# Kernel optimization log

Measured on AMD Instinct MI355X. Metric: run time of the kernel, lower is better.

Reference implementation:

```python
import jax, jax.numpy as jnp
import numpy as np

N = 50000      # nodes
E = 800000     # edges
IN = 128       # in_dim
H = 8          # heads
C = 16         # h_dim (per-head out channels)
ED = 16        # edge_dim
G = 1000       # number of graphs
HC = H * C     # 128
EPS = 1e-16    # PyG softmax epsilon


def setup_inputs() -> dict:
    key = jax.random.key(0)
    ks = jax.random.split(key, 32)
    p = lambda i, shape: jax.random.normal(ks[i], shape, jnp.float32) * 0.1
    inp = {
        "x": jax.random.normal(ks[0], (N, IN), jnp.float32),
        "edge_index": jax.random.randint(ks[1], (2, E), 0, N),
        "edge_attr": jax.random.normal(ks[2], (E, ED), jnp.float32),
        "batch": jnp.sort(jax.random.randint(ks[3], (N,), 0, G)),
    }
    dims = [IN, HC, HC]
    for l in range(3):
        d = dims[l]
        inp[f"W{l+1}"] = p(4 + 6 * l, (d, HC))     # lin weight
        inp[f"We{l+1}"] = p(5 + 6 * l, (ED, HC))   # lin_edge weight
        inp[f"as{l+1}"] = p(6 + 6 * l, (H, C))     # att_src
        inp[f"ad{l+1}"] = p(7 + 6 * l, (H, C))     # att_dst
        inp[f"ae{l+1}"] = p(8 + 6 * l, (H, C))     # att_edge
        inp[f"b{l+1}"] = jnp.zeros((HC,), jnp.float32)
    D = 4 * HC  # cat(h1,h2,h3,h_pool_) -> 512
    inp["Wl1"] = p(22, (D, D)); inp["bl1"] = jnp.zeros((D,), jnp.float32)
    inp["Wl2"] = p(23, (D, 1)); inp["bl2"] = jnp.zeros((1,), jnp.float32)
    return inp


def gat_conv(x, src, dst, edge_attr, W, We, a_s, a_d, a_e, b):
    # x: [N, d_in] -> xs: [N, H, C]
    xs = (x @ W).reshape(-1, H, C)
    ea = (edge_attr @ We).reshape(-1, H, C)          # [E, H, C]
    al_src = jnp.sum(xs * a_s, axis=-1)              # [N, H]
    al_dst = jnp.sum(xs * a_d, axis=-1)              # [N, H]
    al_e = jnp.sum(ea * a_e, axis=-1)                # [E, H]
    alpha = al_src[src] + al_dst[dst] + al_e         # [E, H]
    alpha = jax.nn.leaky_relu(alpha, 0.2)
    amax = jax.ops.segment_max(alpha, dst, num_segments=N)
    ex = jnp.exp(alpha - amax[dst])
    denom = jax.ops.segment_sum(ex, dst, num_segments=N)
    alpha = ex / (denom[dst] + EPS)                  # softmax over in-edges of dst
    msg = xs[src] * alpha[..., None]                 # [E, H, C]
    out = jax.ops.segment_sum(msg, dst, num_segments=N)  # [N, H, C]
    return out.reshape(-1, HC) + b


def reference(x, edge_index, edge_attr, batch,
              W1, We1, as1, ad1, ae1, b1,
              W2, We2, as2, ad2, ae2, b2,
              W3, We3, as3, ad3, ae3, b3,
              Wl1, bl1, Wl2, bl2):
    src, dst = edge_index[0], edge_index[1]
    h1 = gat_conv(x, src, dst, edge_attr, W1, We1, as1, ad1, ae1, b1)
    h2 = gat_conv(h1, src, dst, edge_attr, W2, We2, as2, ad2, ae2, b2)
    h3 = gat_conv(h2, src, dst, edge_attr, W3, We3, as3, ad3, ae3, b3)
    # global_add_pool then broadcast back per node (vectorized gather,
    # replacing the original per-node python loop)
    h_pool = jax.ops.segment_sum(h3, batch, num_segments=G)   # [G, HC]
    h_pool_ = h_pool[batch]                                    # [N, HC]
    h = jnp.concatenate([h1, h2, h3, h_pool_], axis=1)         # [N, 4*HC]
    h = jax.nn.leaky_relu(h @ Wl1 + bl1, 0.01)
    return h @ Wl2 + bl2
```

## Files before the change

kernel.cpp:

```cpp
#include <hip/hip_runtime.h>

#define N_NODES 50000
#define N_EDGES 800000
#define N_GRAPH 1000

typedef short bf16x8 __attribute__((ext_vector_type(8)));
typedef float f32x4 __attribute__((ext_vector_type(4)));

__device__ inline short f2b(float f) {
    union { float f; unsigned u; } x; x.f = f;
    unsigned r = x.u + 0x7FFF + ((x.u >> 16) & 1);
    return (short)(r >> 16);
}
__device__ inline float b2f_lo(unsigned v) {
    union { unsigned u; float f; } x; x.u = v << 16; return x.f;
}
__device__ inline float b2f_hi(unsigned v) {
    union { unsigned u; float f; } x; x.u = v & 0xFFFF0000u; return x.f;
}
__device__ inline float b2f_s(short s) {
    union { unsigned u; float f; } x; x.u = ((unsigned)(unsigned short)s) << 16; return x.f;
}
__device__ inline unsigned pack2(short lo, short hi) {
    return ((unsigned)(unsigned short)lo) | (((unsigned)(unsigned short)hi) << 16);
}

__global__ void f2b_bulk(const float* __restrict__ in, short* __restrict__ out, int n4) {
    int t = blockIdx.x * blockDim.x + threadIdx.x;
    if (t >= n4) return;
    float4 v = *(const float4*)(in + (size_t)t * 4);
    *(short4*)(out + (size_t)t * 4) = make_short4(f2b(v.x), f2b(v.y), f2b(v.z), f2b(v.w));
}

__global__ void wbt_k(const float* __restrict__ W, short* __restrict__ WbT) {
    int idx = blockIdx.x * blockDim.x + threadIdx.x;
    int k = idx >> 7, c = idx & 127;
    WbT[(size_t)c * 128 + k] = f2b(W[idx]);
}

__global__ __launch_bounds__(256) void gemm_mfma(const short* __restrict__ Ab,
                                                 const short* __restrict__ WbT,
                                                 float* __restrict__ out,
                                                 short* __restrict__ outb, int nrows) {
    const int tid = threadIdx.x;
    const int n0 = blockIdx.x * 64;
    const int wid = tid >> 6, lane = tid & 63;
    const int lr = lane & 15, kg = lane >> 4;
    const int wr = (wid >> 1) * 32;
    const int wc = (wid & 1) * 64;

    f32x4 acc[2][4] = {};

#pragma unroll
    for (int ks = 0; ks < 4; ks++) {
        const int k0 = ks * 32;
        bf16x8 a[2], b[4];
#pragma unroll
        for (int fm = 0; fm < 2; fm++) {
            int gr = n0 + wr + fm * 16 + lr;
            bf16x8 v = {};
            if (gr < nrows) v = *(const bf16x8*)(Ab + (size_t)gr * 128 + k0 + kg * 8);
            a[fm] = v;
        }
#pragma unroll
        for (int fn = 0; fn < 4; fn++)
            b[fn] = *(const bf16x8*)(WbT + (size_t)(wc + fn * 16 + lr) * 128 + k0 + kg * 8);
#pragma unroll
        for (int fm = 0; fm < 2; fm++)
#pragma unroll
            for (int fn = 0; fn < 4; fn++)
                acc[fm][fn] = __builtin_amdgcn_mfma_f32_16x16x32_bf16(
                    a[fm], b[fn], acc[fm][fn], 0, 0, 0);
    }
#pragma unroll
    for (int fm = 0; fm < 2; fm++) {
#pragma unroll
        for (int r = 0; r < 4; r++) {
            int gr = n0 + wr + fm * 16 + kg * 4 + r;
            if (gr < nrows) {
#pragma unroll
                for (int fn = 0; fn < 4; fn++) {
                    int col = wc + fn * 16 + lr;
                    float z = acc[fm][fn][r];
                    out[(size_t)gr * 128 + col] = z;
                    outb[(size_t)gr * 128 + col] = f2b(z);
                }
            }
        }
    }
}

__global__ void node_al(const float* __restrict__ xs, const float* __restrict__ a_s,
                        const float* __restrict__ a_d, float* __restrict__ alsrc,
                        float* __restrict__ aldst, int n) {
    int t = blockIdx.x * blockDim.x + threadIdx.x;
    if (t >= n * 8) return;
    int node = t >> 3, h = t & 7;
    const float4* xp = (const float4*)(xs + (size_t)node * 128 + h * 16);
    const float4* sp = (const float4*)(a_s + h * 16);
    const float4* dp = (const float4*)(a_d + h * 16);
    float ss = 0.f, dd = 0.f;
#pragma unroll
    for (int q = 0; q < 4; q++) {
        float4 x4 = xp[q], s4 = sp[q], d4 = dp[q];
        ss += x4.x * s4.x + x4.y * s4.y + x4.z * s4.z + x4.w * s4.w;
        dd += x4.x * d4.x + x4.y * d4.y + x4.z * d4.z + x4.w * d4.w;
    }
    alsrc[t] = ss;
    aldst[t] = dd;
}

__global__ void aew_k(const float* __restrict__ We, const float* __restrict__ ae,
                      float* __restrict__ aeW) {
    int t = threadIdx.x;
    int k = t >> 3, h = t & 7;
    float s = 0.f;
#pragma unroll
    for (int c = 0; c < 16; c++) s += We[k * 128 + h * 16 + c] * ae[h * 16 + c];
    aeW[k * 8 + h] = s;
}

__global__ void hist_k(const int* __restrict__ ei, int* __restrict__ cnt, int ne) {
    int e = blockIdx.x * blockDim.x + threadIdx.x;
    if (e < ne) atomicAdd(&cnt[ei[ne + e]], 1);
}

__global__ void scan1_k(const int* __restrict__ cnt, int* __restrict__ rowptr,
                        int* __restrict__ part, int n) {
    __shared__ int s[256];
    int tid = threadIdx.x;
    int i = blockIdx.x * 256 + tid;
    int v = (i < n) ? cnt[i] : 0;
    s[tid] = v; __syncthreads();
#pragma unroll
    for (int off = 1; off < 256; off <<= 1) {
        int t = (tid >= off) ? s[tid - off] : 0;
        __syncthreads();
        s[tid] += t;
        __syncthreads();
    }
    if (i < n) rowptr[i] = s[tid] - v;
    if (tid == 255) part[blockIdx.x] = s[255];
}

__global__ void scan2_k(int* __restrict__ part, int npart) {
    __shared__ int s[256];
    int tid = threadIdx.x;
    int v = (tid < npart) ? part[tid] : 0;
    s[tid] = v; __syncthreads();
#pragma unroll
    for (int off = 1; off < 256; off <<= 1) {
        int t = (tid >= off) ? s[tid - off] : 0;
        __syncthreads();
        s[tid] += t;
        __syncthreads();
    }
    if (tid < npart) part[tid] = s[tid] - v;
}

__global__ void scan3_k(int* __restrict__ rowptr, const int* __restrict__ part,
                        int* __restrict__ cursor, int n, int ne) {
    int i = blockIdx.x * 256 + threadIdx.x;
    if (i < n) {
        int r = rowptr[i] + part[blockIdx.x];
        rowptr[i] = r;
        cursor[i] = r;
    }
    if (i == 0) rowptr[n] = ne;
}

__global__ void scatter_k(const int* __restrict__ ei, int* __restrict__ cursor,
                          int* __restrict__ pos, int* __restrict__ csr_src, int ne) {
    int e = blockIdx.x * blockDim.x + threadIdx.x;
    if (e >= ne) return;
    int d = ei[ne + e];
    int p = atomicAdd(&cursor[d], 1);
    pos[e] = p;
    csr_src[p] = ei[e];
}

__global__ __launch_bounds__(256) void ale_k(const int* __restrict__ ei,
                                             const float* __restrict__ eattr,
                                             const float* __restrict__ alsrc,
                                             const float* __restrict__ aeW,
                                             const int* __restrict__ pos,
                                             short* __restrict__ aleb, int ne) {
    __shared__ float sAe[128];
    if (threadIdx.x < 128) sAe[threadIdx.x] = aeW[threadIdx.x];
    __syncthreads();
    int e = blockIdx.x * blockDim.x + threadIdx.x;
    if (e >= ne) return;
    float ea[16];
    const float4* ep = (const float4*)(eattr + (size_t)e * 16);
#pragma unroll
    for (int q = 0; q < 4; q++) {
        float4 v = ep[q];
        ea[q * 4 + 0] = v.x; ea[q * 4 + 1] = v.y; ea[q * 4 + 2] = v.z; ea[q * 4 + 3] = v.w;
    }
    int s = ei[e];
    float out[8];
#pragma unroll
    for (int h = 0; h < 8; h++) out[h] = alsrc[s * 8 + h];
#pragma unroll
    for (int k = 0; k < 16; k++)
#pragma unroll
        for (int h = 0; h < 8; h++) out[h] += ea[k] * sAe[k * 8 + h];
    short v8[8];
#pragma unroll
    for (int h = 0; h < 8; h++) v8[h] = f2b(out[h]);
    short* op = aleb + (size_t)pos[e] * 8;
    *(short4*)(op)     = make_short4(v8[0], v8[1], v8[2], v8[3]);
    *(short4*)(op + 4) = make_short4(v8[4], v8[5], v8[6], v8[7]);
}

__global__ __launch_bounds__(256) void gather_k(const int* __restrict__ rowptr,
                                                const int* __restrict__ csr_src,
                                                const short* __restrict__ aleb,
                                                const float* __restrict__ aldst,
                                                const short* __restrict__ xsb,
                                                const float* __restrict__ b,
                                                short* __restrict__ houtb, int n) {
    int dst = blockIdx.x * 4 + (threadIdx.x >> 6);
    if (dst >= n) return;
    const int lane = threadIdx.x & 63;
    const int h = lane >> 3;
    const float L2E = 1.44269504f;
    int p0 = rowptr[dst], p1 = rowptr[dst + 1];
    float ald = aldst[dst * 8 + h];
    float den = 0.f, acc0 = 0.f, acc1 = 0.f;
    int p = p0;
    for (; p + 8 <= p1; p += 8) {
        int   sv  = csr_src[p + (lane & 7)];
        float alv = b2f_s(aleb[(size_t)p * 8 + lane]);
        int s0 = __shfl(sv, 0), s1 = __shfl(sv, 1), s2 = __shfl(sv, 2), s3 = __shfl(sv, 3);
        int s4 = __shfl(sv, 4), s5 = __shfl(sv, 5), s6 = __shfl(sv, 6), s7 = __shfl(sv, 7);
        unsigned v0 = *(const unsigned*)(xsb + (size_t)s0 * 128 + lane * 2);
        unsigned v1 = *(const unsigned*)(xsb + (size_t)s1 * 128 + lane * 2);
        unsigned v2 = *(const unsigned*)(xsb + (size_t)s2 * 128 + lane * 2);
        unsigned v3 = *(const unsigned*)(xsb + (size_t)s3 * 128 + lane * 2);
        unsigned v4 = *(const unsigned*)(xsb + (size_t)s4 * 128 + lane * 2);
        unsigned v5 = *(const unsigned*)(xsb + (size_t)s5 * 128 + lane * 2);
        unsigned v6 = *(const unsigned*)(xsb + (size_t)s6 * 128 + lane * 2);
        unsigned v7 = *(const unsigned*)(xsb + (size_t)s7 * 128 + lane * 2);
        unsigned vv[8] = {v0, v1, v2, v3, v4, v5, v6, v7};
#pragma unroll
        for (int i = 0; i < 8; i++) {
            float al = __shfl(alv, i * 8 + h);
            float lg = al + ald; lg = lg > 0.f ? lg : 0.2f * lg;
            float ex = exp2f(lg * L2E);
            den  += ex;
            acc0 += b2f_lo(vv[i]) * ex;
            acc1 += b2f_hi(vv[i]) * ex;
        }
    }
    for (; p + 1 < p1; p += 2) {
        int s0 = csr_src[p];
        int s1 = csr_src[p + 1];
        float al0 = b2f_s(aleb[(size_t)p * 8 + h]);
        float al1 = b2f_s(aleb[(size_t)(p + 1) * 8 + h]);
        unsigned v0 = *(const unsigned*)(xsb + (size_t)s0 * 128 + lane * 2);
        unsigned v1 = *(const unsigned*)(xsb + (size_t)s1 * 128 + lane * 2);
        float lg0 = al0 + ald; lg0 = lg0 > 0.f ? lg0 : 0.2f * lg0;
        float lg1 = al1 + ald; lg1 = lg1 > 0.f ? lg1 : 0.2f * lg1;
        float ex0 = exp2f(lg0 * L2E);
        float ex1 = exp2f(lg1 * L2E);
        den  += ex0 + ex1;
        acc0 += b2f_lo(v0) * ex0 + b2f_lo(v1) * ex1;
        acc1 += b2f_hi(v0) * ex0 + b2f_hi(v1) * ex1;
    }
    if (p < p1) {
        int s0 = csr_src[p];
        float al0 = b2f_s(aleb[(size_t)p * 8 + h]);
        unsigned v0 = *(const unsigned*)(xsb + (size_t)s0 * 128 + lane * 2);
        float lg0 = al0 + ald; lg0 = lg0 > 0.f ? lg0 : 0.2f * lg0;
        float ex0 = exp2f(lg0 * L2E);
        den  += ex0;
        acc0 += b2f_lo(v0) * ex0;
        acc1 += b2f_hi(v0) * ex0;
    }
    float inv = 1.f / (den + 1e-16f);
    const float2 bb = *(const float2*)(b + lane * 2);
    unsigned o = pack2(f2b(acc0 * inv + bb.x), f2b(acc1 * inv + bb.y));
    *(unsigned*)(houtb + (size_t)dst * 128 + lane * 2) = o;
}

__global__ void pool_k(const short* __restrict__ h3b, const int* __restrict__ batch,
                       float* __restrict__ pool, int n) {
    int t = blockIdx.x * blockDim.x + threadIdx.x;
    if (t >= n * 128) return;
    int node = t >> 7, j = t & 127;
    atomicAdd(pool + (size_t)batch[node] * 128 + j, b2f_s(h3b[t]));
}

__global__ void wl1t_k(const float* __restrict__ Wl1, short* __restrict__ Wl1T) {
    int idx = blockIdx.x * blockDim.x + threadIdx.x;
    int k = idx >> 9, c = idx & 511;
    Wl1T[(size_t)c * 512 + k] = f2b(Wl1[idx]);
}

__global__ void init_out(float* __restrict__ out, const float* __restrict__ bl2, int n) {
    int t = blockIdx.x * blockDim.x + threadIdx.x;
    if (t < n) out[t] = bl2[0];
}

__global__ __launch_bounds__(256) void final_mfma(
    const short* __restrict__ h1, const short* __restrict__ h2,
    const short* __restrict__ h3, const short* __restrict__ poolb,
    const int* __restrict__ batch, const short* __restrict__ Wl1T,
    const float* __restrict__ bl1, const float* __restrict__ Wl2,
    float* __restrict__ out, int nrows)
{
    __shared__ short Abuf[2][4 * 64 * 8];
    __shared__ int   sBatch[64];
    const int tid = threadIdx.x;
    const int n0 = blockIdx.x * 64;
    const int j0 = blockIdx.y * 256;
    const int wid = tid >> 6, lane = tid & 63;
    const int lr = lane & 15, kg = lane >> 4;

    if (tid < 64) {
        int gr = n0 + tid;
        sBatch[tid] = (gr < nrows) ? batch[gr] : 0;
    }
    __syncthreads();

    const short* seg_base[4] = {h1, h2, h3, poolb};

    auto STAGE = [&](int t) {
        const int k0 = t * 32;
        const int seg = k0 >> 7;
        const short* base = seg_base[seg];
        const int cseg = k0 & 127;
        int gr = n0 + lane;
        int grow = (seg == 3) ? sBatch[lane] : ((gr < nrows) ? gr : 0);
        const short* src = base + (size_t)grow * 128 + cseg + wid * 8;
#if __has_builtin(__builtin_amdgcn_global_load_lds)
        __builtin_amdgcn_global_load_lds(
            (const __attribute__((address_space(1))) unsigned int*)src,
            (__attribute__((address_space(3))) unsigned int*)&Abuf[t & 1][(wid * 64 + lane) * 8],
            16, 0, 0);
#else
        uint4 v = *(const uint4*)src;
        *(uint4*)(&Abuf[t & 1][(wid * 64 + lane) * 8]) = v;
#endif
    };
    auto LOADB = [&](int t, bf16x8* bb) {
        const int k0 = t * 32;
#pragma unroll
        for (int fn = 0; fn < 4; fn++)
            bb[fn] = *(const bf16x8*)(Wl1T + (size_t)(j0 + wid * 64 + fn * 16 + lr) * 512
                                      + k0 + kg * 8);
    };

    f32x4 acc[4][4] = {};
    bf16x8 bc[4], bn[4];

    STAGE(0);
    LOADB(0, bc);
    __syncthreads();
#pragma unroll
    for (int t = 0; t < 16; t++) {
        if (t < 15) {
            STAGE(t + 1);
            LOADB(t + 1, bn);
        }
        bf16x8 a[4];
#pragma unroll
        for (int fm = 0; fm < 4; fm++)
            a[fm] = *(const bf16x8*)(&Abuf[t & 1][(kg * 64 + fm * 16 + lr) * 8]);
#pragma unroll
        for (int fm = 0; fm < 4; fm++)
#pragma unroll
            for (int fn = 0; fn < 4; fn++)
                acc[fm][fn] = __builtin_amdgcn_mfma_f32_16x16x32_bf16(
                    a[fm], bc[fn], acc[fm][fn], 0, 0, 0);
        if (t < 15) {
            __syncthreads();
#pragma unroll
            for (int fn = 0; fn < 4; fn++) bc[fn] = bn[fn];
        }
    }

    float w2[4], b1c[4];
#pragma unroll
    for (int fn = 0; fn < 4; fn++) {
        int c = j0 + wid * 64 + fn * 16 + lr;
        w2[fn]  = Wl2[c];
        b1c[fn] = bl1[c];
    }

#pragma unroll
    for (int fm = 0; fm < 4; fm++) {
#pragma unroll
        for (int r = 0; r < 4; r++) {
            float s = 0.f;
#pragma unroll
            for (int fn = 0; fn < 4; fn++) {
                float z = acc[fm][fn][r] + b1c[fn];
                z = z > 0.f ? z : 0.01f * z;
                s += z * w2[fn];
            }
            s += __shfl_xor(s, 1);
            s += __shfl_xor(s, 2);
            s += __shfl_xor(s, 4);
            s += __shfl_xor(s, 8);
            if (lr == 0) {
                int gr = n0 + fm * 16 + kg * 4 + r;
                if (gr < nrows) atomicAdd(out + gr, s);
            }
        }
    }
}

extern "C" void kernel_launch(void* const* d_in, const int* in_sizes, int n_in,
                              void* d_out, int out_size, void* d_ws, size_t ws_size,
                              hipStream_t stream) {
    const float* x     = (const float*)d_in[0];
    const int*   ei    = (const int*)d_in[1];
    const float* eattr = (const float*)d_in[2];
    const int*   batch = (const int*)d_in[3];
    const float* W[3]   = {(const float*)d_in[4],  (const float*)d_in[10], (const float*)d_in[16]};
    const float* We[3]  = {(const float*)d_in[5],  (const float*)d_in[11], (const float*)d_in[17]};
    const float* as_[3] = {(const float*)d_in[6],  (const float*)d_in[12], (const float*)d_in[18]};
    const float* ad_[3] = {(const float*)d_in[7],  (const float*)d_in[13], (const float*)d_in[19]};
    const float* ae_[3] = {(const float*)d_in[8],  (const float*)d_in[14], (const float*)d_in[20]};
    const float* b_[3]  = {(const float*)d_in[9],  (const float*)d_in[15], (const float*)d_in[21]};
    const float* Wl1 = (const float*)d_in[22];
    const float* bl1 = (const float*)d_in[23];
    const float* Wl2 = (const float*)d_in[24];
    const float* bl2 = (const float*)d_in[25];

    const int N = N_NODES, E = N_EDGES, G = N_GRAPH;

    float* ws    = (float*)d_ws;
    float* xs    = ws;
    float* alsrc = xs + (size_t)N * 128;
    float* aldst = alsrc + (size_t)N * 8;
    float* pool  = aldst + (size_t)N * 8;
    float* aeW   = pool + (size_t)G * 128;
    short* xb    = (short*)(aeW + 128);
    short* xsb   = xb + (size_t)N * 128;
    short* hb0   = xsb + (size_t)N * 128;
    short* hb1   = hb0 + (size_t)N * 128;
    short* hb2   = hb1 + (size_t)N * 128;
    short* hb[3] = {hb0, hb1, hb2};
    short* poolb = hb2 + (size_t)N * 128;
    short* wbt0  = poolb + (size_t)G * 128;
    short* wbt1  = wbt0 + 16384;
    short* wbt2  = wbt1 + 16384;
    short* wbt[3] = {wbt0, wbt1, wbt2};
    short* wl1t  = wbt2 + 16384;
    short* aleb  = wl1t + 262144;
    int*   cnt     = (int*)(aleb + (size_t)E * 8);
    int*   rowptr  = cnt + N;
    int*   cursor  = rowptr + N + 1;
    int*   part    = cursor + N;
    int*   pos     = part + 256;
    int*   csr_src = pos + E;

    f2b_bulk<<<(N * 32 + 255) / 256, 256, 0, stream>>>(x, xb, N * 32);
    for (int l = 0; l < 3; l++)
        wbt_k<<<64, 256, 0, stream>>>(W[l], wbt[l]);
    wl1t_k<<<1024, 256, 0, stream>>>(Wl1, wl1t);
    hipMemsetAsync(cnt, 0, (size_t)N * sizeof(int), stream);
    hist_k<<<(E + 255) / 256, 256, 0, stream>>>(ei, cnt, E);
    const int nblk = (N + 255) / 256;
    scan1_k<<<nblk, 256, 0, stream>>>(cnt, rowptr, part, N);
    scan2_k<<<1, 256, 0, stream>>>(part, nblk);
    scan3_k<<<nblk, 256, 0, stream>>>(rowptr, part, cursor, N, E);
    scatter_k<<<(E + 255) / 256, 256, 0, stream>>>(ei, cursor, pos, csr_src, E);

    for (int l = 0; l < 3; l++) {
        const short* Ain = (l == 0) ? xb : hb[l - 1];
        gemm_mfma<<<(N + 63) / 64, 256, 0, stream>>>(Ain, wbt[l], xs, xsb, N);
        node_al<<<(N * 8 + 255) / 256, 256, 0, stream>>>(xs, as_[l], ad_[l], alsrc, aldst, N);
        aew_k<<<1, 128, 0, stream>>>(We[l], ae_[l], aeW);
        ale_k<<<(E + 255) / 256, 256, 0, stream>>>(ei, eattr, alsrc, aeW, pos, aleb, E);
        gather_k<<<(N + 3) / 4, 256, 0, stream>>>(rowptr, csr_src, aleb, aldst, xsb,
                                                  b_[l], hb[l], N);
    }
    hipMemsetAsync(pool, 0, (size_t)G * 128 * sizeof(float), stream);
    pool_k<<<(N * 128 + 255) / 256, 256, 0, stream>>>(hb[2], batch, pool, N);
    f2b_bulk<<<(G * 32 + 255) / 256, 256, 0, stream>>>(pool, poolb, G * 32);

    init_out<<<(N + 255) / 256, 256, 0, stream>>>((float*)d_out, bl2, N);
    dim3 fg((N + 63) / 64, 2);
    final_mfma<<<fg, 256, 0, stream>>>(hb[0], hb[1], hb[2], poolb, batch,
                                       wl1t, bl1, Wl2, (float*)d_out, N);
}
```

Measured before the change: 487.6 us.

## Drop fp32 GEMM output, fold aeW into ale_k, prefetch gather edges

The GEMM now writes only the bf16 projection, and node_al computes attention logits from that bf16 copy. This removes the fp32 store and reload of a 50000x128 buffer in each layer. The tiny aew_k launch is removed by having every ale_k block recompute the 16x8 edge-attention projection into shared memory. The gather loop now software-prefetches the next chunk of source indices and edge logits to hide load latency. The cost is slightly lower precision in the logits and redundant per-block computation of the projection.

```diff
diff --git a/kernel.cpp b/kernel.cpp
--- a/kernel.cpp
+++ b/kernel.cpp
@@ -40,7 +40,6 @@
 
 __global__ __launch_bounds__(256) void gemm_mfma(const short* __restrict__ Ab,
                                                  const short* __restrict__ WbT,
-                                                 float* __restrict__ out,
                                                  short* __restrict__ outb, int nrows) {
     const int tid = threadIdx.x;
     const int n0 = blockIdx.x * 64;
@@ -81,43 +80,32 @@
 #pragma unroll
                 for (int fn = 0; fn < 4; fn++) {
                     int col = wc + fn * 16 + lr;
-                    float z = acc[fm][fn][r];
-                    out[(size_t)gr * 128 + col] = z;
-                    outb[(size_t)gr * 128 + col] = f2b(z);
+                    outb[(size_t)gr * 128 + col] = f2b(acc[fm][fn][r]);
                 }
             }
         }
     }
 }
 
-__global__ void node_al(const float* __restrict__ xs, const float* __restrict__ a_s,
+__global__ void node_al(const short* __restrict__ xsb, const float* __restrict__ a_s,
                         const float* __restrict__ a_d, float* __restrict__ alsrc,
                         float* __restrict__ aldst, int n) {
     int t = blockIdx.x * blockDim.x + threadIdx.x;
     if (t >= n * 8) return;
     int node = t >> 3, h = t & 7;
-    const float4* xp = (const float4*)(xs + (size_t)node * 128 + h * 16);
-    const float4* sp = (const float4*)(a_s + h * 16);
-    const float4* dp = (const float4*)(a_d + h * 16);
+    const short* xp = xsb + (size_t)node * 128 + h * 16;
+    uint4 u0 = *(const uint4*)(xp);
+    uint4 u1 = *(const uint4*)(xp + 8);
+    unsigned w[8] = {u0.x, u0.y, u0.z, u0.w, u1.x, u1.y, u1.z, u1.w};
     float ss = 0.f, dd = 0.f;
 #pragma unroll
-    for (int q = 0; q < 4; q++) {
-        float4 x4 = xp[q], s4 = sp[q], d4 = dp[q];
-        ss += x4.x * s4.x + x4.y * s4.y + x4.z * s4.z + x4.w * s4.w;
-        dd += x4.x * d4.x + x4.y * d4.y + x4.z * d4.z + x4.w * d4.w;
+    for (int q = 0; q < 8; q++) {
+        float lo = b2f_lo(w[q]), hi = b2f_hi(w[q]);
+        ss += lo * a_s[h * 16 + q * 2] + hi * a_s[h * 16 + q * 2 + 1];
+        dd += lo * a_d[h * 16 + q * 2] + hi * a_d[h * 16 + q * 2 + 1];
     }
     alsrc[t] = ss;
     aldst[t] = dd;
-}
-
-__global__ void aew_k(const float* __restrict__ We, const float* __restrict__ ae,
-                      float* __restrict__ aeW) {
-    int t = threadIdx.x;
-    int k = t >> 3, h = t & 7;
-    float s = 0.f;
-#pragma unroll
-    for (int c = 0; c < 16; c++) s += We[k * 128 + h * 16 + c] * ae[h * 16 + c];
-    aeW[k * 8 + h] = s;
 }
 
 __global__ void hist_k(const int* __restrict__ ei, int* __restrict__ cnt, int ne) {
@@ -182,11 +170,18 @@
 __global__ __launch_bounds__(256) void ale_k(const int* __restrict__ ei,
                                              const float* __restrict__ eattr,
                                              const float* __restrict__ alsrc,
-                                             const float* __restrict__ aeW,
+                                             const float* __restrict__ We,
+                                             const float* __restrict__ ae,
                                              const int* __restrict__ pos,
                                              short* __restrict__ aleb, int ne) {
     __shared__ float sAe[128];
-    if (threadIdx.x < 128) sAe[threadIdx.x] = aeW[threadIdx.x];
+    if (threadIdx.x < 128) {
+        int k = threadIdx.x >> 3, h = threadIdx.x & 7;
+        float s = 0.f;
+#pragma unroll
+        for (int c = 0; c < 16; c++) s += We[k * 128 + h * 16 + c] * ae[h * 16 + c];
+        sAe[threadIdx.x] = s;
+    }
     __syncthreads();
     int e = blockIdx.x * blockDim.x + threadIdx.x;
     if (e >= ne) return;
@@ -229,11 +224,22 @@
     float ald = aldst[dst * 8 + h];
     float den = 0.f, acc0 = 0.f, acc1 = 0.f;
     int p = p0;
-    for (; p + 8 <= p1; p += 8) {
-        int   sv  = csr_src[p + (lane & 7)];
-        float alv = b2f_s(aleb[(size_t)p * 8 + lane]);
-        int s0 = __shfl(sv, 0), s1 = __shfl(sv, 1), s2 = __shfl(sv, 2), s3 = __shfl(sv, 3);
-        int s4 = __shfl(sv, 4), s5 = __shfl(sv, 5), s6 = __shfl(sv, 6), s7 = __shfl(sv, 7);
+    const int nfull = (p1 - p0) >> 3;
+    int   sv  = 0;
+    float alv = 0.f;
+    if (nfull > 0) {
+        sv  = csr_src[p + (lane & 7)];
+        alv = b2f_s(aleb[(size_t)p * 8 + lane]);
+    }
+    for (int c = 0; c < nfull; c++) {
+        int csv = sv; float calv = alv;
+        int pn = p + 8;
+        if (c + 1 < nfull) {
+            sv  = csr_src[pn + (lane & 7)];
+            alv = b2f_s(aleb[(size_t)pn * 8 + lane]);
+        }
+        int s0 = __shfl(csv, 0), s1 = __shfl(csv, 1), s2 = __shfl(csv, 2), s3 = __shfl(csv, 3);
+        int s4 = __shfl(csv, 4), s5 = __shfl(csv, 5), s6 = __shfl(csv, 6), s7 = __shfl(csv, 7);
         unsigned v0 = *(const unsigned*)(xsb + (size_t)s0 * 128 + lane * 2);
         unsigned v1 = *(const unsigned*)(xsb + (size_t)s1 * 128 + lane * 2);
         unsigned v2 = *(const unsigned*)(xsb + (size_t)s2 * 128 + lane * 2);
@@ -245,13 +251,14 @@
         unsigned vv[8] = {v0, v1, v2, v3, v4, v5, v6, v7};
 #pragma unroll
         for (int i = 0; i < 8; i++) {
-            float al = __shfl(alv, i * 8 + h);
+            float al = __shfl(calv, i * 8 + h);
             float lg = al + ald; lg = lg > 0.f ? lg : 0.2f * lg;
             float ex = exp2f(lg * L2E);
             den  += ex;
             acc0 += b2f_lo(vv[i]) * ex;
             acc1 += b2f_hi(vv[i]) * ex;
         }
+        p = pn;
     }
     for (; p + 1 < p1; p += 2) {
         int s0 = csr_src[p];
@@ -433,12 +440,10 @@
     const int N = N_NODES, E = N_EDGES, G = N_GRAPH;
 
     float* ws    = (float*)d_ws;
-    float* xs    = ws;
-    float* alsrc = xs + (size_t)N * 128;
+    float* alsrc = ws;
     float* aldst = alsrc + (size_t)N * 8;
     float* pool  = aldst + (size_t)N * 8;
-    float* aeW   = pool + (size_t)G * 128;
-    short* xb    = (short*)(aeW + 128);
+    short* xb    = (short*)(pool + (size_t)G * 128);
     short* xsb   = xb + (size_t)N * 128;
     short* hb0   = xsb + (size_t)N * 128;
     short* hb1   = hb0 + (size_t)N * 128;
@@ -472,10 +477,10 @@
 
     for (int l = 0; l < 3; l++) {
         const short* Ain = (l == 0) ? xb : hb[l - 1];
-        gemm_mfma<<<(N + 63) / 64, 256, 0, stream>>>(Ain, wbt[l], xs, xsb, N);
-        node_al<<<(N * 8 + 255) / 256, 256, 0, stream>>>(xs, as_[l], ad_[l], alsrc, aldst, N);
-        aew_k<<<1, 128, 0, stream>>>(We[l], ae_[l], aeW);
-        ale_k<<<(E + 255) / 256, 256, 0, stream>>>(ei, eattr, alsrc, aeW, pos, aleb, E);
+        gemm_mfma<<<(N + 63) / 64, 256, 0, stream>>>(Ain, wbt[l], xsb, N);
+        node_al<<<(N * 8 + 255) / 256, 256, 0, stream>>>(xsb, as_[l], ad_[l], alsrc, aldst, N);
+        ale_k<<<(E + 255) / 256, 256, 0, stream>>>(ei, eattr, alsrc, We[l], ae_[l],
+                                                   pos, aleb, E);
         gather_k<<<(N + 3) / 4, 256, 0, stream>>>(rowptr, csr_src, aleb, aldst, xsb,
                                                   b_[l], hb[l], N);
     }
```

Result: no change. 482.2 us (-1.1%).
